# Kernel tuning notes

Measured on AMD Instinct MI355X. Metric: run time of the kernel, lower is better.

Reference implementation:

```python
import jax, jax.numpy as jnp
import numpy as np

B, C, H, W = 8, 128, 192, 192
CROP = 39
LEN = CROP // 2            # 19 -> 38x38 crop
CY = CX = 96               # fixed crop center (original draws random.randint(19, 173))
MARGIN = 1.0


def grid_sample_bilinear(img, grid):
    """Bilinear grid_sample, align_corners=True, zeros padding.
    img: (B,C,H,W); grid: (B,H,W,2) with (x,y) in [-1,1]."""
    _, _, Hi, Wi = img.shape
    gx = (grid[..., 0] + 1.0) * 0.5 * (Wi - 1)   # (B,H,W) source x
    gy = (grid[..., 1] + 1.0) * 0.5 * (Hi - 1)   # (B,H,W) source y
    x0 = jnp.floor(gx)
    y0 = jnp.floor(gy)

    def gather(xf, yf):
        valid = (xf >= 0) & (xf <= Wi - 1) & (yf >= 0) & (yf <= Hi - 1)
        xi = jnp.clip(xf, 0, Wi - 1).astype(jnp.int32)
        yi = jnp.clip(yf, 0, Hi - 1).astype(jnp.int32)
        # per-batch gather: (C,H,W) values at integer (y,x) locations
        v = jax.vmap(lambda im, y, x: im[:, y, x])(img, yi, xi)  # (B,C,H,W)
        return v * valid[:, None, :, :].astype(img.dtype)

    wx1 = gx - x0
    wx0 = 1.0 - wx1
    wy1 = gy - y0
    wy0 = 1.0 - wy1
    w = lambda a: a[:, None, :, :]
    return (w(wx0 * wy0) * gather(x0,       y0)
          + w(wx1 * wy0) * gather(x0 + 1.0, y0)
          + w(wx0 * wy1) * gather(x0,       y0 + 1.0)
          + w(wx1 * wy1) * gather(x0 + 1.0, y0 + 1.0))


def hardnet_loss(anchor, positive, margin=MARGIN):
    """loss_HardNet with anchor_swap=False, batch_reduce='min', triplet_margin."""
    d1 = jnp.sum(anchor * anchor, axis=1)                       # (N,)
    d2 = jnp.sum(positive * positive, axis=1)                   # (N,)
    sq = d1[:, None] + d2[None, :] - 2.0 * (anchor @ positive.T)  # (N,N)
    dm = jnp.sqrt(jnp.maximum(sq, 0.0) + 1e-6) + 1e-8
    n = dm.shape[0]
    pos = jnp.diagonal(dm)                                      # positive distances
    dmod = dm + jnp.eye(n, dtype=dm.dtype) * 10.0               # mask diagonal
    dmod = dmod + jnp.where(dmod < 0.008, 10.0, 0.0)            # mask near-duplicates
    min_neg = jnp.min(dmod, axis=1)                             # hardest negative per anchor
    return jnp.mean(jnp.maximum(margin + pos - min_neg, 0.0))


def setup_inputs() -> dict:
    key = jax.random.key(0)
    k1, k2, k3 = jax.random.split(key, 3)
    feat1 = jax.random.normal(k1, (B, C, H, W), dtype=jnp.float32)
    feat2 = jax.random.normal(k2, (B, C, H, W), dtype=jnp.float32)
    # absolute flow: pixel coordinates in [0, W-1] / [0, H-1]
    aflow = jax.random.uniform(k3, (B, 2, H, W), dtype=jnp.float32) * (W - 1)
    return {"feat1": feat1, "feat2": feat2, "aflow": aflow}


def reference(feat1, feat2, aflow):
    # _aflow_to_grid: pixel coords -> [-1,1] grid (align_corners=True convention)
    gx = aflow[:, 0] * (2.0 / (W - 1)) - 1.0
    gy = aflow[:, 1] * (2.0 / (H - 1)) - 1.0
    grid = jnp.stack([gx, gy], axis=-1)                          # (B,H,W,2)
    grid = jnp.where(jnp.isnan(grid), 9e9, grid)                 # invalid -> out of range
    feat2to1 = grid_sample_bilinear(feat2, grid)                 # warp img2 feats to img1
    s = slice(CY - LEN, CY + LEN)                                # fixed 38x38 crop
    f1 = feat1[:, :, s, s]
    f2 = feat2to1[:, :, s, s]
    a = f1.transpose(0, 2, 3, 1).reshape(-1, C)                  # (B*38*38, C)
    p = f2.transpose(0, 2, 3, 1).reshape(-1, C)
    return hardnet_loss(a, p)
```

## Files before the change

### kernel.cpp

```cpp
#include <hip/hip_runtime.h>
#include <stdint.h>

#define Hh 192
#define Ww 192
#define HW 36864
#define CROPW 38
#define CW2 1444
#define CROPOFF 77
#define NPTS 11552
#define NPAD 11776
#define NMT 92
#define NCT 92
#define NG 5
#define JPB 19
#define NBLK (NG*NMT)
#define CROPB 304
#define CRDB 46
#define BIGF 3.0e38f

typedef short bf16x8 __attribute__((ext_vector_type(8)));
typedef float f32x4 __attribute__((ext_vector_type(4)));
typedef uint32_t u32x2 __attribute__((ext_vector_type(2)));
typedef uint32_t u32x4 __attribute__((ext_vector_type(4)));
typedef unsigned short ushort;

__device__ __forceinline__ ushort f2bf(float f) {
  uint32_t b = __float_as_uint(f);
  uint32_t r = b + 0x7fffu + ((b >> 16) & 1u);
  return (ushort)(r >> 16);
}
__device__ __forceinline__ float bf2f(ushort u) {
  return __uint_as_float(((uint32_t)u) << 16);
}

__device__ __forceinline__ void g2l16(const void* g, void* l) {
  __builtin_amdgcn_global_load_lds(
      (const __attribute__((address_space(1))) unsigned int*)g,
      (__attribute__((address_space(3))) unsigned int*)l, 16, 0, 0);
}

__global__ __launch_bounds__(256) void prep2_k(
    const float* __restrict__ feat1, const float* __restrict__ aflow,
    ushort* __restrict__ aB, ushort* __restrict__ pB,
    float* __restrict__ d1, float* __restrict__ d2,
    u32x4* __restrict__ coords) {
  int bid = blockIdx.x;
  int t = threadIdx.x;
  if (bid < CROPB) {
    __shared__ __align__(16) ushort lsh[38*136];
    int b = bid / CROPW, r = bid % CROPW;
    int y = CROPOFF + r;
    {
      int xo = t & 63, c0 = t >> 6;
      if (xo < CROPW) {
        const float* src = feat1 + ((size_t)b*128*HW) + (size_t)y*Ww + CROPOFF + xo;
        #pragma unroll
        for (int k = 0; k < 32; ++k) {
          int cc = c0*32 + k;
          lsh[xo*136 + cc] = f2bf(src[(size_t)cc*HW]);
        }
      }
    }
    __syncthreads();
    int chunk = t & 7, p0 = t >> 3;
    #pragma unroll
    for (int pp = 0; pp < 2; ++pp) {
      int p = p0 + pp*32;
      if (p >= CROPW) break;
      int idx = b*CW2 + r*CROPW + p;
      ushort* dst = aB + (size_t)idx*128 + chunk*16;
      *(bf16x8*)dst       = *(const bf16x8*)&lsh[p*136 + chunk*16];
      *(bf16x8*)(dst + 8) = *(const bf16x8*)&lsh[p*136 + chunk*16 + 8];
      float s = 0.f;
      #pragma unroll
      for (int j = 0; j < 16; ++j) {
        float v = bf2f(lsh[p*136 + chunk*16 + j]);
        s += v*v;
      }
      s += __shfl_xor(s, 1); s += __shfl_xor(s, 2); s += __shfl_xor(s, 4);
      if (chunk == 0) d1[idx] = s;
    }
  } else if (bid < CROPB + CRDB) {
    int idx = (bid - CROPB)*256 + t;
    if (idx >= NPTS) return;
    d2[idx] = 0.f;
    int b = idx / CW2;
    int rem = idx % CW2;
    int r = rem / CROPW, cx = rem % CROPW;
    int y = CROPOFF + r, x = CROPOFF + cx;
    float ax = aflow[((b*2 + 0)*Hh + y)*Ww + x];
    float ay = aflow[((b*2 + 1)*Hh + y)*Ww + x];
    float gxn = ax * (2.0f/(Ww-1)) - 1.0f;
    float gyn = ay * (2.0f/(Hh-1)) - 1.0f;
    float gx = (gxn + 1.0f) * 0.5f * (Ww-1);
    float gy = (gyn + 1.0f) * 0.5f * (Hh-1);
    int xi = min((int)floorf(gx), Ww-2);
    int yi = min((int)floorf(gy), Hh-2);
    u32x4 cd;
    cd.x = (uint32_t)(yi*Ww + xi);
    cd.y = __float_as_uint(gx - (float)xi);
    cd.z = __float_as_uint(gy - (float)yi);
    cd.w = 0;
    coords[idx] = cd;
  } else {
    if (t < NPAD - NPTS) {
      int row = NPTS + t;
      u32x4 z = {0,0,0,0};
      #pragma unroll
      for (int c = 0; c < 8; ++c) {
        *(u32x4*)&aB[(size_t)row*128 + c*16] = z;
        *(u32x4*)&aB[(size_t)row*128 + c*16 + 8] = z;
        *(u32x4*)&pB[(size_t)row*128 + c*16] = z;
        *(u32x4*)&pB[(size_t)row*128 + c*16 + 8] = z;
      }
      d1[row] = 0.f;
      d2[row] = 1e30f;
    }
  }
}

__global__ __launch_bounds__(256) void slab_k(
    const float* __restrict__ feat2, const u32x4* __restrict__ coords,
    ushort* __restrict__ pB, float* __restrict__ d2) {
  __shared__ __align__(16) uint32_t plane[HW];
  int bid = blockIdx.x;
  int b = bid >> 6, cp = bid & 63, c = cp*2;
  int t = threadIdx.x;
  const float* srcA = feat2 + ((size_t)(b*128 + c)) * HW;
  const float* srcB = srcA + HW;
  #pragma unroll 6
  for (int k = 0; k < 36; ++k) {
    int i = (k*256 + t) * 4;
    f32x4 va = *(const f32x4*)(srcA + i);
    f32x4 vb = *(const f32x4*)(srcB + i);
    u32x4 pk;
    #pragma unroll
    for (int j = 0; j < 4; ++j)
      pk[j] = (uint32_t)f2bf(va[j]) | ((uint32_t)f2bf(vb[j]) << 16);
    *(u32x4*)&plane[i] = pk;
  }
  __syncthreads();
  int pbase = b*CW2;
  #pragma unroll
  for (int it = 0; it < 6; ++it) {
    int p = it*256 + t;
    if (p < CW2) {
      u32x4 cd = coords[pbase + p];
      int cell = (int)cd.x;
      float wx1 = __uint_as_float(cd.y), wx0 = 1.f - wx1;
      float wy1 = __uint_as_float(cd.z), wy0 = 1.f - wy1;
      uint32_t u00 = plane[cell];
      uint32_t u01 = plane[cell + 1];
      uint32_t u10 = plane[cell + Ww];
      uint32_t u11 = plane[cell + Ww + 1];
      float v0 = wy0*(wx0*bf2f((ushort)u00) + wx1*bf2f((ushort)u01))
               + wy1*(wx0*bf2f((ushort)u10) + wx1*bf2f((ushort)u11));
      float v1 = wy0*(wx0*bf2f((ushort)(u00>>16)) + wx1*bf2f((ushort)(u01>>16)))
               + wy1*(wx0*bf2f((ushort)(u10>>16)) + wx1*bf2f((ushort)(u11>>16)));
      ushort q0 = f2bf(v0), q1 = f2bf(v1);
      *(uint32_t*)&pB[(size_t)(pbase + p)*128 + c] = (uint32_t)q0 | ((uint32_t)q1 << 16);
      float f0 = bf2f(q0), f1 = bf2f(q1);
      atomicAdd(&d2[pbase + p], f0*f0 + f1*f1);
    }
  }
}

__global__ __launch_bounds__(256) void gemmp_k(
    const ushort* __restrict__ aB, const ushort* __restrict__ pB,
    const float* __restrict__ d1, const float* __restrict__ d2,
    float* __restrict__ pos, float* __restrict__ pmin) {
  __shared__ __align__(16) ushort lB[2][128*128];

  int bid = blockIdx.x;
  int xcd = bid & 7, kk = bid >> 3;
  int start = (xcd < 4) ? xcd*58 : 232 + (xcd-4)*57;
  int L = start + kk;
  int g = L / NMT, tM = L % NMT;
  int j0 = g * JPB;
  int jn = (NCT - j0 < JPB) ? (NCT - j0) : JPB;

  int tid = threadIdx.x;
  int rowg = tid >> 4, cb = (tid & 15) << 4;
  int w = tid >> 6, l = tid & 63;
  int wr = w >> 1, wc = w & 1;
  int lcol = l & 15, hq = l >> 4, rb = hq << 2;
  int rsw = (lcol & 7) << 4;

  {
    const char* gB = (const char*)pB + (size_t)j0 * 128 * 256;
    #pragma unroll
    for (int rnd = 0; rnd < 8; ++rnd) {
      int row = rnd*16 + rowg;
      g2l16(gB + row*256 + (cb ^ ((row&7)<<4)), (char*)lB[0] + row*256 + cb);
    }
  }

  bf16x8 aF[16];
  {
    const char* gA = (const char*)aB + ((size_t)(tM*128 + wr*64 + lcol))*256 + hq*16;
    #pragma unroll
    for (int ma = 0; ma < 4; ++ma)
      #pragma unroll
      for (int ks = 0; ks < 4; ++ks)
        aF[ma*4+ks] = *(const bf16x8*)(gA + ma*16*256 + ks*64);
  }
  __syncthreads();

  float mPart[4] = {BIGF, BIGF, BIGF, BIGF};

  for (int it = 0; it < jn; ++it) {
    int j = j0 + it;
    if (it + 1 < jn) {
      const char* gB = (const char*)pB + (size_t)(j+1) * 128 * 256;
      char* dst = (char*)lB[(it+1) & 1];
      #pragma unroll
      for (int rnd = 0; rnd < 8; ++rnd) {
        int row = rnd*16 + rowg;
        g2l16(gB + row*256 + (cb ^ ((row&7)<<4)), dst + row*256 + cb);
      }
    }
    f32x4 d2v[4];
    #pragma unroll
    for (int np = 0; np < 4; ++np)
      d2v[np] = *(const f32x4*)&d2[j*128 + wc*64 + np*16 + rb];

    const char* bufB = (const char*)lB[it & 1];
    f32x4 acc[4][4] = {};
    #pragma unroll
    for (int ks = 0; ks < 4; ++ks) {
      int cbase = ks*64 + (hq << 4);
      bf16x8 bF[4];
      #pragma unroll
      for (int np = 0; np < 4; ++np)
        bF[np] = *(const bf16x8*)(bufB + (wc*64 + np*16 + lcol)*256 + (cbase ^ rsw));
      #pragma unroll
      for (int np = 0; np < 4; ++np)
        #pragma unroll
        for (int ma = 0; ma < 4; ++ma)
          acc[np][ma] = __builtin_amdgcn_mfma_f32_16x16x32_bf16(bF[np], aF[ma*4+ks], acc[np][ma], 0, 0, 0);
    }

    if (j != tM) {
      #pragma unroll
      for (int ma = 0; ma < 4; ++ma)
        #pragma unroll
        for (int np = 0; np < 4; ++np)
          #pragma unroll
          for (int reg = 0; reg < 4; ++reg)
            mPart[ma] = fminf(mPart[ma], fmaf(-2.f, acc[np][ma][reg], d2v[np][reg]));
    } else {
      #pragma unroll
      for (int ma = 0; ma < 4; ++ma) {
        int gi = tM*128 + wr*64 + ma*16 + lcol;
        #pragma unroll
        for (int np = 0; np < 4; ++np)
          #pragma unroll
          for (int reg = 0; reg < 4; ++reg) {
            int gj = j*128 + wc*64 + np*16 + rb + reg;
            float t = fmaf(-2.f, acc[np][ma][reg], d2v[np][reg]);
            if (gi == gj)
              pos[gi] = sqrtf(fmaxf(d1[gi] + t, 0.f) + 1e-6f) + 1e-8f;
            else
              mPart[ma] = fminf(mPart[ma], t);
          }
      }
    }
    __syncthreads();
  }

  #pragma unroll
  for (int ma = 0; ma < 4; ++ma) {
    float u = mPart[ma];
    u = fminf(u, __shfl_xor(u, 16));
    u = fminf(u, __shfl_xor(u, 32));
    mPart[ma] = u;
  }
  __syncthreads();
  float* sm = (float*)lB;
  if (hq == 0) {
    #pragma unroll
    for (int ma = 0; ma < 4; ++ma)
      sm[wc*128 + wr*64 + ma*16 + lcol] = mPart[ma];
  }
  __syncthreads();
  if (tid < 128) {
    int row = tM*128 + tid;
    float u = fminf(sm[tid], sm[128 + tid]);
    pmin[g*NPAD + row] = sqrtf(fmaxf(d1[row] + u, 0.f) + 1e-6f) + 1e-8f;
  }
}

__global__ __launch_bounds__(1024) void fin_k(const float* __restrict__ pos,
                                              const float* __restrict__ pmin,
                                              float* __restrict__ out) {
  float s = 0.f;
  for (int i = threadIdx.x; i < NPTS; i += 1024) {
    float p = pos[i];
    float mneg = p + 10.f;
    #pragma unroll
    for (int g = 0; g < NG; ++g) mneg = fminf(mneg, pmin[g*NPAD + i]);
    s += fmaxf(1.0f + p - mneg, 0.f);
  }
  for (int off = 1; off < 64; off <<= 1) s += __shfl_xor(s, off);
  __shared__ float red[16];
  if ((threadIdx.x & 63) == 0) red[threadIdx.x >> 6] = s;
  __syncthreads();
  if (threadIdx.x == 0) {
    float t = 0.f;
    #pragma unroll
    for (int k = 0; k < 16; ++k) t += red[k];
    out[0] = t / (float)NPTS;
  }
}

extern "C" void kernel_launch(void* const* d_in, const int* in_sizes, int n_in,
                              void* d_out, int out_size, void* d_ws, size_t ws_size,
                              hipStream_t stream) {
  const float* feat1 = (const float*)d_in[0];
  const float* feat2 = (const float*)d_in[1];
  const float* aflow = (const float*)d_in[2];

  char* ws = (char*)d_ws;
  ushort* aB = (ushort*)ws;
  ushort* pB = aB + (size_t)NPAD * 128;
  float*  d1 = (float*)(pB + (size_t)NPAD * 128);
  float*  d2 = d1 + NPAD;
  float*  pos = d2 + NPAD;
  float*  pmin = pos + NPAD;
  u32x4*  coords = (u32x4*)(pmin + (size_t)NG*NPAD);

  hipLaunchKernelGGL(prep2_k, dim3(CROPB + CRDB + 1), dim3(256), 0, stream,
                     feat1, aflow, aB, pB, d1, d2, coords);
  hipLaunchKernelGGL(slab_k, dim3(512), dim3(256), 0, stream,
                     feat2, coords, pB, d2);
  hipLaunchKernelGGL(gemmp_k, dim3(NBLK), dim3(256), 0, stream,
                     aB, pB, d1, d2, pos, pmin);
  hipLaunchKernelGGL(fin_k, dim3(1), dim3(1024), 0, stream,
                     pos, pmin, (float*)d_out);
}
```

Before: 93.72 us.

## Fuse crop prep and bilinear slab sampling into one 1024-thread kernel

Merges the prep kernel and the slab warp kernel into a single launch with 1024-thread blocks. Slab blocks now compute sampling coordinates inline from aflow instead of reading a precomputed coords buffer, so the coords round trip and one kernel boundary go away. Zeroing of d2 moves to a hipMemsetAsync ahead of the kernel. Every block now reserves the full 144KB LDS plane, including the crop blocks, and the larger blocks change occupancy and per-thread work.

```diff
diff --git a/kernel.cpp b/kernel.cpp
--- a/kernel.cpp
+++ b/kernel.cpp
@@ -14,13 +14,12 @@
 #define NG 5
 #define JPB 19
 #define NBLK (NG*NMT)
+#define SLABB 512
 #define CROPB 304
-#define CRDB 46
 #define BIGF 3.0e38f
 
 typedef short bf16x8 __attribute__((ext_vector_type(8)));
 typedef float f32x4 __attribute__((ext_vector_type(4)));
-typedef uint32_t u32x2 __attribute__((ext_vector_type(2)));
 typedef uint32_t u32x4 __attribute__((ext_vector_type(4)));
 typedef unsigned short ushort;
 
@@ -39,34 +38,82 @@
       (__attribute__((address_space(3))) unsigned int*)l, 16, 0, 0);
 }
 
-__global__ __launch_bounds__(256) void prep2_k(
-    const float* __restrict__ feat1, const float* __restrict__ aflow,
+__global__ __launch_bounds__(1024) void fused_k(
+    const float* __restrict__ feat1, const float* __restrict__ feat2,
+    const float* __restrict__ aflow,
     ushort* __restrict__ aB, ushort* __restrict__ pB,
-    float* __restrict__ d1, float* __restrict__ d2,
-    u32x4* __restrict__ coords) {
+    float* __restrict__ d1, float* __restrict__ d2) {
+  __shared__ __align__(16) uint32_t plane[HW];
   int bid = blockIdx.x;
   int t = threadIdx.x;
-  if (bid < CROPB) {
-    __shared__ __align__(16) ushort lsh[38*136];
-    int b = bid / CROPW, r = bid % CROPW;
+
+  if (bid < SLABB) {
+    int b = bid >> 6, c = (bid & 63) * 2;
+    const float* srcA = feat2 + ((size_t)(b*128 + c)) * HW;
+    const float* srcB = srcA + HW;
+    #pragma unroll
+    for (int k = 0; k < 9; ++k) {
+      int i = (k*1024 + t) * 4;
+      f32x4 va = *(const f32x4*)(srcA + i);
+      f32x4 vb = *(const f32x4*)(srcB + i);
+      u32x4 pk;
+      #pragma unroll
+      for (int j = 0; j < 4; ++j)
+        pk[j] = (uint32_t)f2bf(va[j]) | ((uint32_t)f2bf(vb[j]) << 16);
+      *(u32x4*)&plane[i] = pk;
+    }
+    __syncthreads();
+    int pbase = b*CW2;
+    #pragma unroll
+    for (int it = 0; it < 2; ++it) {
+      int p = it*1024 + t;
+      if (p < CW2) {
+        int r = p / CROPW, cx = p % CROPW;
+        int y = CROPOFF + r, x = CROPOFF + cx;
+        float ax = aflow[((b*2 + 0)*Hh + y)*Ww + x];
+        float ay = aflow[((b*2 + 1)*Hh + y)*Ww + x];
+        float gxn = ax * (2.0f/(Ww-1)) - 1.0f;
+        float gyn = ay * (2.0f/(Hh-1)) - 1.0f;
+        float gx = (gxn + 1.0f) * 0.5f * (Ww-1);
+        float gy = (gyn + 1.0f) * 0.5f * (Hh-1);
+        int xi = min((int)floorf(gx), Ww-2);
+        int yi = min((int)floorf(gy), Hh-2);
+        float wx1 = gx - (float)xi, wx0 = 1.f - wx1;
+        float wy1 = gy - (float)yi, wy0 = 1.f - wy1;
+        int cell = yi*Ww + xi;
+        uint32_t u00 = plane[cell];
+        uint32_t u01 = plane[cell + 1];
+        uint32_t u10 = plane[cell + Ww];
+        uint32_t u11 = plane[cell + Ww + 1];
+        float v0 = wy0*(wx0*bf2f((ushort)u00) + wx1*bf2f((ushort)u01))
+                 + wy1*(wx0*bf2f((ushort)u10) + wx1*bf2f((ushort)u11));
+        float v1 = wy0*(wx0*bf2f((ushort)(u00>>16)) + wx1*bf2f((ushort)(u01>>16)))
+                 + wy1*(wx0*bf2f((ushort)(u10>>16)) + wx1*bf2f((ushort)(u11>>16)));
+        ushort q0 = f2bf(v0), q1 = f2bf(v1);
+        *(uint32_t*)&pB[(size_t)(pbase + p)*128 + c] = (uint32_t)q0 | ((uint32_t)q1 << 16);
+        float f0 = bf2f(q0), f1 = bf2f(q1);
+        atomicAdd(&d2[pbase + p], f0*f0 + f1*f1);
+      }
+    }
+  } else if (bid < SLABB + CROPB) {
+    ushort* lsh = (ushort*)plane;
+    int rb2 = bid - SLABB;
+    int b = rb2 / CROPW, r = rb2 % CROPW;
     int y = CROPOFF + r;
     {
-      int xo = t & 63, c0 = t >> 6;
+      int xo = t & 63, cg = t >> 6;
       if (xo < CROPW) {
         const float* src = feat1 + ((size_t)b*128*HW) + (size_t)y*Ww + CROPOFF + xo;
         #pragma unroll
-        for (int k = 0; k < 32; ++k) {
-          int cc = c0*32 + k;
+        for (int k = 0; k < 8; ++k) {
+          int cc = cg + k*16;
           lsh[xo*136 + cc] = f2bf(src[(size_t)cc*HW]);
         }
       }
     }
     __syncthreads();
-    int chunk = t & 7, p0 = t >> 3;
-    #pragma unroll
-    for (int pp = 0; pp < 2; ++pp) {
-      int p = p0 + pp*32;
-      if (p >= CROPW) break;
+    int chunk = t & 7, p = t >> 3;
+    if (p < CROPW) {
       int idx = b*CW2 + r*CROPW + p;
       ushort* dst = aB + (size_t)idx*128 + chunk*16;
       *(bf16x8*)dst       = *(const bf16x8*)&lsh[p*136 + chunk*16];
@@ -80,28 +127,6 @@
       s += __shfl_xor(s, 1); s += __shfl_xor(s, 2); s += __shfl_xor(s, 4);
       if (chunk == 0) d1[idx] = s;
     }
-  } else if (bid < CROPB + CRDB) {
-    int idx = (bid - CROPB)*256 + t;
-    if (idx >= NPTS) return;
-    d2[idx] = 0.f;
-    int b = idx / CW2;
-    int rem = idx % CW2;
-    int r = rem / CROPW, cx = rem % CROPW;
-    int y = CROPOFF + r, x = CROPOFF + cx;
-    float ax = aflow[((b*2 + 0)*Hh + y)*Ww + x];
-    float ay = aflow[((b*2 + 1)*Hh + y)*Ww + x];
-    float gxn = ax * (2.0f/(Ww-1)) - 1.0f;
-    float gyn = ay * (2.0f/(Hh-1)) - 1.0f;
-    float gx = (gxn + 1.0f) * 0.5f * (Ww-1);
-    float gy = (gyn + 1.0f) * 0.5f * (Hh-1);
-    int xi = min((int)floorf(gx), Ww-2);
-    int yi = min((int)floorf(gy), Hh-2);
-    u32x4 cd;
-    cd.x = (uint32_t)(yi*Ww + xi);
-    cd.y = __float_as_uint(gx - (float)xi);
-    cd.z = __float_as_uint(gy - (float)yi);
-    cd.w = 0;
-    coords[idx] = cd;
   } else {
     if (t < NPAD - NPTS) {
       int row = NPTS + t;
@@ -115,52 +140,6 @@
       }
       d1[row] = 0.f;
       d2[row] = 1e30f;
-    }
-  }
-}
-
-__global__ __launch_bounds__(256) void slab_k(
-    const float* __restrict__ feat2, const u32x4* __restrict__ coords,
-    ushort* __restrict__ pB, float* __restrict__ d2) {
-  __shared__ __align__(16) uint32_t plane[HW];
-  int bid = blockIdx.x;
-  int b = bid >> 6, cp = bid & 63, c = cp*2;
-  int t = threadIdx.x;
-  const float* srcA = feat2 + ((size_t)(b*128 + c)) * HW;
-  const float* srcB = srcA + HW;
-  #pragma unroll 6
-  for (int k = 0; k < 36; ++k) {
-    int i = (k*256 + t) * 4;
-    f32x4 va = *(const f32x4*)(srcA + i);
-    f32x4 vb = *(const f32x4*)(srcB + i);
-    u32x4 pk;
-    #pragma unroll
-    for (int j = 0; j < 4; ++j)
-      pk[j] = (uint32_t)f2bf(va[j]) | ((uint32_t)f2bf(vb[j]) << 16);
-    *(u32x4*)&plane[i] = pk;
-  }
-  __syncthreads();
-  int pbase = b*CW2;
-  #pragma unroll
-  for (int it = 0; it < 6; ++it) {
-    int p = it*256 + t;
-    if (p < CW2) {
-      u32x4 cd = coords[pbase + p];
-      int cell = (int)cd.x;
-      float wx1 = __uint_as_float(cd.y), wx0 = 1.f - wx1;
-      float wy1 = __uint_as_float(cd.z), wy0 = 1.f - wy1;
-      uint32_t u00 = plane[cell];
-      uint32_t u01 = plane[cell + 1];
-      uint32_t u10 = plane[cell + Ww];
-      uint32_t u11 = plane[cell + Ww + 1];
-      float v0 = wy0*(wx0*bf2f((ushort)u00) + wx1*bf2f((ushort)u01))
-               + wy1*(wx0*bf2f((ushort)u10) + wx1*bf2f((ushort)u11));
-      float v1 = wy0*(wx0*bf2f((ushort)(u00>>16)) + wx1*bf2f((ushort)(u01>>16)))
-               + wy1*(wx0*bf2f((ushort)(u10>>16)) + wx1*bf2f((ushort)(u11>>16)));
-      ushort q0 = f2bf(v0), q1 = f2bf(v1);
-      *(uint32_t*)&pB[(size_t)(pbase + p)*128 + c] = (uint32_t)q0 | ((uint32_t)q1 << 16);
-      float f0 = bf2f(q0), f1 = bf2f(q1);
-      atomicAdd(&d2[pbase + p], f0*f0 + f1*f1);
     }
   }
 }
@@ -327,12 +306,10 @@
   float*  d2 = d1 + NPAD;
   float*  pos = d2 + NPAD;
   float*  pmin = pos + NPAD;
-  u32x4*  coords = (u32x4*)(pmin + (size_t)NG*NPAD);
-
-  hipLaunchKernelGGL(prep2_k, dim3(CROPB + CRDB + 1), dim3(256), 0, stream,
-                     feat1, aflow, aB, pB, d1, d2, coords);
-  hipLaunchKernelGGL(slab_k, dim3(512), dim3(256), 0, stream,
-                     feat2, coords, pB, d2);
+
+  hipMemsetAsync(d2, 0, NPTS * sizeof(float), stream);
+  hipLaunchKernelGGL(fused_k, dim3(SLABB + CROPB + 1), dim3(1024), 0, stream,
+                     feat1, feat2, aflow, aB, pB, d1, d2);
   hipLaunchKernelGGL(gemmp_k, dim3(NBLK), dim3(256), 0, stream,
                      aB, pB, d1, d2, pos, pmin);
   hipLaunchKernelGGL(fin_k, dim3(1), dim3(1024), 0, stream,
```

After: 89.96 us. 1.04x faster.
